# Optimization experiments

Hardware: AMD Instinct MI355X
Metric: run time of the kernel (lower is better)

The kernel has to match this reference:

```python
import jax, jax.numpy as jnp
import numpy as np

# HashGrid config (from ExplicitMaterial.Config defaults)
N_LEVELS = 16
F_PER_LEVEL = 2
TABLE_SIZE = 1 << 19          # log2_hashmap_size = 19
BASE_RES = 16
GROWTH = 1.447269237440378
N_NEURONS = 64                # VanillaMLP hidden width
N_OUT = 3                     # n_output_dims
N_POINTS = 1048576

# 8 trilinear corner offsets, [8,3]
OFFSETS = np.stack(np.meshgrid([0, 1], [0, 1], [0, 1], indexing='ij'), -1).reshape(8, 3)
PRIMES = np.array([1, 2654435761, 805459861], dtype=np.uint32)  # tcnn spatial hash primes


def _level_params():
    # tcnn convention: scale = base * growth^l - 1, resolution = ceil(scale) + 1
    out = []
    for l in range(N_LEVELS):
        scale = BASE_RES * (GROWTH ** l) - 1.0
        res = int(np.ceil(scale)) + 1
        out.append((scale, res))
    return out


def hash_grid_encode(x01, table):
    # x01: [N,3] in [0,1]; table: [L, T, F]
    offsets_u = jnp.asarray(OFFSETS, dtype=jnp.uint32)          # [8,3]
    offsets_f = jnp.asarray(OFFSETS, dtype=x01.dtype)           # [8,3]
    outs = []
    for l, (scale, res) in enumerate(_level_params()):
        pos = x01 * scale + 0.5                                  # [N,3]
        p0f = jnp.floor(pos)
        frac = pos - p0f                                         # [N,3]
        p0 = p0f.astype(jnp.uint32)
        corners = p0[:, None, :] + offsets_u                     # [N,8,3]
        if res ** 3 <= TABLE_SIZE:
            # dense indexing for coarse levels
            c = jnp.minimum(corners, np.uint32(res - 1))
            idx = c[..., 0] + c[..., 1] * np.uint32(res) + c[..., 2] * np.uint32(res * res)
        else:
            # spatial hash: xor of coordinate * prime, masked to table size
            idx = (corners[..., 0] * np.uint32(PRIMES[0])) \
                ^ (corners[..., 1] * np.uint32(PRIMES[1])) \
                ^ (corners[..., 2] * np.uint32(PRIMES[2]))
            idx = idx & np.uint32(TABLE_SIZE - 1)
        feats = table[l][idx]                                    # [N,8,F] gather
        w = jnp.prod(jnp.where(offsets_f[None] > 0, frac[:, None, :], 1.0 - frac[:, None, :]), axis=-1)  # [N,8]
        outs.append(jnp.sum(w[..., None] * feats, axis=1))       # [N,F]
    return jnp.concatenate(outs, axis=-1)                        # [N, L*F]


def setup_inputs() -> dict:
    key = jax.random.key(0)
    k1, k2, k3, k4 = jax.random.split(key, 4)
    positions = jax.random.uniform(k1, (N_POINTS, 3), dtype=jnp.float32, minval=-1.0, maxval=1.0)
    # tcnn init: uniform(-1e-4, 1e-4)
    hash_table = jax.random.uniform(k2, (N_LEVELS, TABLE_SIZE, F_PER_LEVEL), dtype=jnp.float32,
                                    minval=-1e-4, maxval=1e-4)
    d_in = N_LEVELS * F_PER_LEVEL
    w1 = jax.random.normal(k3, (d_in, N_NEURONS), dtype=jnp.float32) * (2.0 / d_in) ** 0.5
    w2 = jax.random.normal(k4, (N_NEURONS, N_OUT), dtype=jnp.float32) * (2.0 / N_NEURONS) ** 0.5
    return {"positions": positions, "hash_table": hash_table, "w1": w1, "w2": w2}


def reference(positions, hash_table, w1, w2):
    # contract_to_unisphere (bounded): scale bbox [-1,1]^3 -> [0,1]^3
    x01 = (positions + 1.0) * 0.5
    enc = hash_grid_encode(x01, hash_table)                      # [N,32]
    h = jax.nn.relu(enc @ w1)                                    # VanillaMLP, bias-free
    feat = h @ w2                                                # output_activation = none
    color = jax.nn.sigmoid(feat)                                 # material_activation
    return color
```

## Files before the change

### kernel.cpp

```cpp
#include <hip/hip_runtime.h>
#include <stdint.h>
#include <math.h>

#define NLEVELS 16
#define NDENSE  5
#define NHASH   11
#define TSIZE   (1u << 19)
#define HMASK   (TSIZE - 1u)
#define PRIME_Y 2654435761u
#define PRIME_Z 805459861u

#define FP8_SCALE 8192.0f
#define FP8_INV   (1.0f / 8192.0f)

typedef float v2f __attribute__((ext_vector_type(2)));

struct Params {
    float    scale[NLEVELS];
    unsigned res[NDENSE];
    unsigned doff[NDENSE];
    unsigned dmode;
};

__device__ __forceinline__ unsigned umin_(unsigned a, unsigned b) { return a < b ? a : b; }

__device__ __forceinline__ v2f fma2(float w, v2f f, v2f a) {
    v2f wv = {w, w};
    return __builtin_elementwise_fma(wv, f, a);
}

__global__ __launch_bounds__(256) void repack_hash8(const float4* __restrict__ src,
                                                    uint2* __restrict__ dst, int n4) {
    const int i = blockIdx.x * 256 + threadIdx.x;
    if (i >= n4) return;
    const float4 a = src[2 * i];
    const float4 b = src[2 * i + 1];
    int lo = __builtin_amdgcn_cvt_pk_fp8_f32(a.x * FP8_SCALE, a.y * FP8_SCALE, 0, false);
    lo     = __builtin_amdgcn_cvt_pk_fp8_f32(a.z * FP8_SCALE, a.w * FP8_SCALE, lo, true);
    int hi = __builtin_amdgcn_cvt_pk_fp8_f32(b.x * FP8_SCALE, b.y * FP8_SCALE, 0, false);
    hi     = __builtin_amdgcn_cvt_pk_fp8_f32(b.z * FP8_SCALE, b.w * FP8_SCALE, hi, true);
    dst[i] = make_uint2((unsigned)lo, (unsigned)hi);
}

__global__ __launch_bounds__(256) void repack_dense8(const float2* __restrict__ table,
                                                     uint2* __restrict__ dst, Params pr) {
    const int l = blockIdx.y;
    const unsigned R = pr.res[l];
    const unsigned n = R * R * R;
    const unsigned e = blockIdx.x * 256 + threadIdx.x;
    if (e >= n) return;
    const unsigned xx = e % R;
    const unsigned t  = e / R;
    const unsigned yy = t % R;
    const unsigned x1 = umin_(xx + 1u, R - 1) - xx;
    const unsigned y1 = (umin_(yy + 1u, R - 1) - yy) * R;
    const float2* src = table + (size_t)l * TSIZE;
    const float2 a = src[e];
    const float2 b = src[e + x1];
    const float2 c = src[e + y1];
    const float2 d = src[e + y1 + x1];
    int w0 = __builtin_amdgcn_cvt_pk_fp8_f32(a.x * FP8_SCALE, a.y * FP8_SCALE, 0, false);
    w0     = __builtin_amdgcn_cvt_pk_fp8_f32(b.x * FP8_SCALE, b.y * FP8_SCALE, w0, true);
    int w1 = __builtin_amdgcn_cvt_pk_fp8_f32(c.x * FP8_SCALE, c.y * FP8_SCALE, 0, false);
    w1     = __builtin_amdgcn_cvt_pk_fp8_f32(d.x * FP8_SCALE, d.y * FP8_SCALE, w1, true);
    dst[pr.doff[l] + e] = make_uint2((unsigned)w0, (unsigned)w1);
}

__global__ __launch_bounds__(256) void repack_dense16(const float2* __restrict__ table,
                                                      uint4* __restrict__ dst, Params pr) {
    const int l = blockIdx.y;
    const unsigned R = pr.res[l];
    const unsigned n = R * R * R;
    const unsigned e = blockIdx.x * 256 + threadIdx.x;
    if (e >= n) return;
    const unsigned xx = e % R;
    const unsigned t  = e / R;
    const unsigned yy = t % R;
    const unsigned zz = t / R;
    const unsigned x1 = umin_(xx + 1u, R - 1) - xx;
    const unsigned y1 = (umin_(yy + 1u, R - 1) - yy) * R;
    const unsigned z1 = (umin_(zz + 1u, R - 1) - zz) * R * R;
    const float2* src = table + (size_t)l * TSIZE;
    const float2 a0 = src[e];
    const float2 b0 = src[e + x1];
    const float2 c0 = src[e + y1];
    const float2 d0 = src[e + y1 + x1];
    const float2 a1 = src[e + z1];
    const float2 b1 = src[e + z1 + x1];
    const float2 c1 = src[e + z1 + y1];
    const float2 d1 = src[e + z1 + y1 + x1];
    int w0 = __builtin_amdgcn_cvt_pk_fp8_f32(a0.x * FP8_SCALE, a0.y * FP8_SCALE, 0, false);
    w0     = __builtin_amdgcn_cvt_pk_fp8_f32(b0.x * FP8_SCALE, b0.y * FP8_SCALE, w0, true);
    int w1 = __builtin_amdgcn_cvt_pk_fp8_f32(c0.x * FP8_SCALE, c0.y * FP8_SCALE, 0, false);
    w1     = __builtin_amdgcn_cvt_pk_fp8_f32(d0.x * FP8_SCALE, d0.y * FP8_SCALE, w1, true);
    int w2 = __builtin_amdgcn_cvt_pk_fp8_f32(a1.x * FP8_SCALE, a1.y * FP8_SCALE, 0, false);
    w2     = __builtin_amdgcn_cvt_pk_fp8_f32(b1.x * FP8_SCALE, b1.y * FP8_SCALE, w2, true);
    int w3 = __builtin_amdgcn_cvt_pk_fp8_f32(c1.x * FP8_SCALE, c1.y * FP8_SCALE, 0, false);
    w3     = __builtin_amdgcn_cvt_pk_fp8_f32(d1.x * FP8_SCALE, d1.y * FP8_SCALE, w3, true);
    uint4 o; o.x = (unsigned)w0; o.y = (unsigned)w1; o.z = (unsigned)w2; o.w = (unsigned)w3;
    dst[pr.doff[l] + e] = o;
}

__device__ __forceinline__ void lvl_tw(float x, float y, float z, float s,
                                       float* wx, float* wy, float* wz) {
    const float fx = fmaf(x, s, 0.5f), fy = fmaf(y, s, 0.5f), fz = fmaf(z, s, 0.5f);
    const float tx = fx - floorf(fx), ty = fy - floorf(fy), tz = fz - floorf(fz);
    wx[0] = 1.f - tx; wx[1] = tx;
    wy[0] = 1.f - ty; wy[1] = ty;
    wz[0] = 1.f - tz; wz[1] = tz;
}

__device__ __forceinline__ void hash_issue_pair(const void* __restrict__ hashTV, int lrel,
                                                float x, float y, float z, float s,
                                                unsigned* __restrict__ U,
                                                unsigned* __restrict__ V,
                                                unsigned* __restrict__ flg) {
    const float fx = fmaf(x, s, 0.5f), fy = fmaf(y, s, 0.5f), fz = fmaf(z, s, 0.5f);
    const unsigned x0 = (unsigned)floorf(fx);
    const unsigned y0 = (unsigned)floorf(fy);
    const unsigned z0 = (unsigned)floorf(fz);
    const unsigned hy0 = y0 * PRIME_Y, hz0 = z0 * PRIME_Z;
    unsigned H[4];
    H[0] = hy0 ^ hz0;
    H[1] = (hy0 + PRIME_Y) ^ hz0;
    H[2] = hy0 ^ (hz0 + PRIME_Z);
    H[3] = (hy0 + PRIME_Y) ^ (hz0 + PRIME_Z);
    *flg = (x0 & 1u) | (((y0 ^ z0) & 1u) << 1);
    if (x0 & 1u) {
        const unsigned short* t8 = (const unsigned short*)hashTV + (size_t)lrel * TSIZE;
#pragma unroll
        for (int c = 0; c < 4; ++c) {
            const unsigned i0 = (x0 ^ H[c]) & HMASK;
            const unsigned i1 = ((x0 + 1u) ^ H[c]) & HMASK;
            U[c] = t8[i0];
            V[c] = t8[i1];
        }
    } else {
        const unsigned* t32 = (const unsigned*)hashTV + (size_t)lrel * (TSIZE / 2);
#pragma unroll
        for (int c = 0; c < 4; ++c) {
            const unsigned i0 = (x0 ^ H[c]) & HMASK;
            U[c] = t32[i0 >> 1];
        }
    }
}

__global__ __launch_bounds__(256) void hgmlp_fp8p(
    const float* __restrict__ gpos,
    const void* __restrict__ hashTV,
    const void* __restrict__ denseTV,
    const float* __restrict__ gw1,
    const float* __restrict__ gw2,
    float* __restrict__ gout,
    int npts, Params pr)
{
    __shared__ __align__(16) float w1t[64 * 32];
    __shared__ float w2s[64 * 3];
    __shared__ __align__(16) float ostage[768];
    const int tid = threadIdx.x;
    const int p = blockIdx.x * 256 + tid;
    const bool full = (blockIdx.x * 256 + 256) <= npts;

    float px = 0.f, py = 0.f, pz = 0.f;
    if (p < npts) { px = gpos[3 * p]; py = gpos[3 * p + 1]; pz = gpos[3 * p + 2]; }

    for (int e = tid; e < 32 * 64; e += 256) {
        const int i = e & 31, j = e >> 5;
        w1t[e] = gw1[i * 64 + j] * FP8_INV;
    }
    if (tid < 192) w2s[tid] = gw2[tid];
    __syncthreads();

    const float x = (px + 1.f) * 0.5f;
    const float y = (py + 1.f) * 0.5f;
    const float z = (pz + 1.f) * 0.5f;

    v2f enc[16];

    uint4 dq[NDENSE];
#pragma unroll
    for (int l = 0; l < NDENSE; ++l) {
        const float s = pr.scale[l];
        const unsigned R = pr.res[l];
        const float fx = fmaf(x, s, 0.5f), fy = fmaf(y, s, 0.5f), fz = fmaf(z, s, 0.5f);
        const unsigned x0 = (unsigned)floorf(fx);
        const unsigned y0 = (unsigned)floorf(fy);
        const unsigned z0 = (unsigned)floorf(fz);
        const unsigned base = umin_(x0, R - 1) + umin_(y0, R - 1) * R
                            + umin_(z0, R - 1) * R * R;
        if (pr.dmode) {
            const uint4* tl = (const uint4*)denseTV + pr.doff[l];
            dq[l] = tl[base];
        } else {
            const unsigned cz1 = umin_(z0 + 1u, R - 1) * R * R - umin_(z0, R - 1) * R * R;
            const uint2* tl = (const uint2*)denseTV + pr.doff[l];
            const uint2 u0 = tl[base];
            const uint2 u1 = tl[base + cz1];
            dq[l].x = u0.x; dq[l].y = u0.y; dq[l].z = u1.x; dq[l].w = u1.y;
        }
    }

    unsigned U[4][4], V[4][4], flg[4];
    hash_issue_pair(hashTV, 0, x, y, z, pr.scale[5], U[0], V[0], &flg[0]);
    hash_issue_pair(hashTV, 1, x, y, z, pr.scale[6], U[1], V[1], &flg[1]);
    hash_issue_pair(hashTV, 2, x, y, z, pr.scale[7], U[2], V[2], &flg[2]);

#pragma unroll
    for (int l = 0; l < NDENSE; ++l) {
        float wx[2], wy[2], wz[2];
        lvl_tw(x, y, z, pr.scale[l], wx, wy, wz);
        v2f e = {0.f, 0.f};
        {
            const v2f c00 = __builtin_amdgcn_cvt_pk_f32_fp8((int)dq[l].x, false);
            const v2f c10 = __builtin_amdgcn_cvt_pk_f32_fp8((int)dq[l].x, true);
            const v2f c01 = __builtin_amdgcn_cvt_pk_f32_fp8((int)dq[l].y, false);
            const v2f c11 = __builtin_amdgcn_cvt_pk_f32_fp8((int)dq[l].y, true);
            e = fma2(wz[0] * wy[0] * wx[0], c00, e);
            e = fma2(wz[0] * wy[0] * wx[1], c10, e);
            e = fma2(wz[0] * wy[1] * wx[0], c01, e);
            e = fma2(wz[0] * wy[1] * wx[1], c11, e);
        }
        {
            const v2f c00 = __builtin_amdgcn_cvt_pk_f32_fp8((int)dq[l].z, false);
            const v2f c10 = __builtin_amdgcn_cvt_pk_f32_fp8((int)dq[l].z, true);
            const v2f c01 = __builtin_amdgcn_cvt_pk_f32_fp8((int)dq[l].w, false);
            const v2f c11 = __builtin_amdgcn_cvt_pk_f32_fp8((int)dq[l].w, true);
            e = fma2(wz[1] * wy[0] * wx[0], c00, e);
            e = fma2(wz[1] * wy[0] * wx[1], c10, e);
            e = fma2(wz[1] * wy[1] * wx[0], c01, e);
            e = fma2(wz[1] * wy[1] * wx[1], c11, e);
        }
        enc[l] = e;
    }

#pragma unroll
    for (int l = NDENSE; l < NLEVELS; ++l) {
        if (l + 3 < NLEVELS) {
            const int sl = (l + 3 - NDENSE) & 3;
            hash_issue_pair(hashTV, l + 3 - NDENSE, x, y, z, pr.scale[l + 3],
                            U[sl], V[sl], &flg[sl]);
        }
        const int sl = (l - NDENSE) & 3;
        float wx[2], wy[2], wz[2];
        lvl_tw(x, y, z, pr.scale[l], wx, wy, wz);
        const unsigned xo = flg[sl] & 1u;
        const unsigned pb = (flg[sl] >> 1) & 1u;
        v2f e = {0.f, 0.f};
#pragma unroll
        for (int c = 0; c < 4; ++c) {
            const unsigned u = U[sl][c];
            const unsigned lo = u & 0xFFFFu, hi = u >> 16;
            const unsigned swp = (xo ^ 1u) & (pb ^ (unsigned)(c & 1) ^ (unsigned)(c >> 1));
            const unsigned ec0 = xo ? lo : (swp ? hi : lo);
            const unsigned ec1 = xo ? (V[sl][c] & 0xFFFFu) : (swp ? lo : hi);
            const v2f f0 = __builtin_amdgcn_cvt_pk_f32_fp8((int)ec0, false);
            const v2f f1 = __builtin_amdgcn_cvt_pk_f32_fp8((int)ec1, false);
            const float wc = wy[c & 1] * wz[c >> 1];
            e = fma2(wc * wx[0], f0, e);
            e = fma2(wc * wx[1], f1, e);
        }
        enc[l] = e;
    }

    float o0 = 0.f, o1 = 0.f, o2 = 0.f;
#pragma unroll 4
    for (int j = 0; j < 64; ++j) {
        const float4* wr4 = (const float4*)&w1t[j * 32];
        v2f a0 = {0.f, 0.f}, a1 = {0.f, 0.f};
#pragma unroll
        for (int i = 0; i < 8; ++i) {
            const float4 w4 = wr4[i];
            const v2f wlo = {w4.x, w4.y};
            const v2f whi = {w4.z, w4.w};
            a0 = __builtin_elementwise_fma(enc[2 * i],     wlo, a0);
            a1 = __builtin_elementwise_fma(enc[2 * i + 1], whi, a1);
        }
        float acc = (a0.x + a0.y) + (a1.x + a1.y);
        acc = fmaxf(acc, 0.f);
        o0 = fmaf(acc, w2s[3 * j + 0], o0);
        o1 = fmaf(acc, w2s[3 * j + 1], o1);
        o2 = fmaf(acc, w2s[3 * j + 2], o2);
    }
    const float r0 = 1.f / (1.f + __expf(-o0));
    const float r1 = 1.f / (1.f + __expf(-o1));
    const float r2 = 1.f / (1.f + __expf(-o2));

    if (full) {
        ostage[3 * tid + 0] = r0;
        ostage[3 * tid + 1] = r1;
        ostage[3 * tid + 2] = r2;
        __syncthreads();
        if (tid < 192) {
            const float4 v = ((const float4*)ostage)[tid];
            ((float4*)(gout + (size_t)blockIdx.x * 768))[tid] = v;
        }
    } else if (p < npts) {
        gout[3 * p + 0] = r0;
        gout[3 * p + 1] = r1;
        gout[3 * p + 2] = r2;
    }
}

__global__ __launch_bounds__(256) void hgmlp_fp32(
    const float* __restrict__ gpos, const float* __restrict__ gtable,
    const float* __restrict__ gw1, const float* __restrict__ gw2,
    float* __restrict__ gout, int npts, Params pr)
{
    __shared__ float w1t[64 * 32];
    __shared__ float w2s[64 * 3];
    const int tid = threadIdx.x;
    const int p = blockIdx.x * 256 + tid;
    float px = 0.f, py = 0.f, pz = 0.f;
    if (p < npts) { px = gpos[3 * p]; py = gpos[3 * p + 1]; pz = gpos[3 * p + 2]; }
    for (int e = tid; e < 32 * 64; e += 256) { const int i = e & 31, j = e >> 5; w1t[e] = gw1[i * 64 + j]; }
    if (tid < 192) w2s[tid] = gw2[tid];
    __syncthreads();
    if (p >= npts) return;
    const float x = (px + 1.f) * 0.5f, y = (py + 1.f) * 0.5f, z = (pz + 1.f) * 0.5f;
    float enc[32];
#pragma unroll
    for (int l = 0; l < NLEVELS; ++l) {
        const float s = pr.scale[l];
        const float fx = fmaf(x, s, 0.5f), fy = fmaf(y, s, 0.5f), fz = fmaf(z, s, 0.5f);
        const float bx = floorf(fx), by = floorf(fy), bz = floorf(fz);
        const float tx = fx - bx, ty = fy - by, tz = fz - bz;
        const unsigned x0 = (unsigned)bx, y0 = (unsigned)by, z0 = (unsigned)bz;
        const float wx[2] = {1.f - tx, tx}, wy[2] = {1.f - ty, ty}, wz[2] = {1.f - tz, tz};
        const float2* tl = (const float2*)gtable + (size_t)l * TSIZE;
        float e0 = 0.f, e1 = 0.f;
        unsigned idx[8];
        if (l < NDENSE) {
            const unsigned R = pr.res[l];
            const unsigned cx[2] = {umin_(x0, R - 1), umin_(x0 + 1u, R - 1)};
            const unsigned cy[2] = {umin_(y0, R - 1) * R, umin_(y0 + 1u, R - 1) * R};
            const unsigned cz[2] = {umin_(z0, R - 1) * R * R, umin_(z0 + 1u, R - 1) * R * R};
#pragma unroll
            for (int c = 0; c < 8; ++c) idx[c] = cx[c & 1] + cy[(c >> 1) & 1] + cz[c >> 2];
        } else {
            const unsigned hy0 = y0 * PRIME_Y, hz0 = z0 * PRIME_Z;
#pragma unroll
            for (int c = 0; c < 8; ++c)
                idx[c] = ((x0 + (c & 1)) ^ (hy0 + ((c >> 1) & 1) * PRIME_Y) ^ (hz0 + (c >> 2) * PRIME_Z)) & HMASK;
        }
#pragma unroll
        for (int c = 0; c < 8; ++c) {
            const float2 f = tl[idx[c]];
            const float w = wx[c & 1] * wy[(c >> 1) & 1] * wz[c >> 2];
            e0 = fmaf(w, f.x, e0); e1 = fmaf(w, f.y, e1);
        }
        enc[2 * l + 0] = e0; enc[2 * l + 1] = e1;
    }
    float o0 = 0.f, o1 = 0.f, o2 = 0.f;
    for (int j = 0; j < 64; ++j) {
        const float* wr = &w1t[j * 32];
        float acc = 0.f;
#pragma unroll
        for (int i = 0; i < 32; ++i) acc = fmaf(enc[i], wr[i], acc);
        acc = fmaxf(acc, 0.f);
        o0 = fmaf(acc, w2s[3 * j + 0], o0);
        o1 = fmaf(acc, w2s[3 * j + 1], o1);
        o2 = fmaf(acc, w2s[3 * j + 2], o2);
    }
    gout[3 * p + 0] = 1.f / (1.f + __expf(-o0));
    gout[3 * p + 1] = 1.f / (1.f + __expf(-o1));
    gout[3 * p + 2] = 1.f / (1.f + __expf(-o2));
}

extern "C" void kernel_launch(void* const* d_in, const int* in_sizes, int n_in,
                              void* d_out, int out_size, void* d_ws, size_t ws_size,
                              hipStream_t stream)
{
    const float* gpos   = (const float*)d_in[0];
    const float* gtable = (const float*)d_in[1];
    const float* gw1    = (const float*)d_in[2];
    const float* gw2    = (const float*)d_in[3];
    float* gout = (float*)d_out;
    const int npts = in_sizes[0] / 3;

    Params pr;
    unsigned total = 0, maxn = 0;
    for (int l = 0; l < NLEVELS; ++l) {
        const double scale = 16.0 * pow(1.447269237440378, (double)l) - 1.0;
        pr.scale[l] = (float)scale;
        if (l < NDENSE) {
            const unsigned R = (unsigned)ceil(scale) + 1u;
            pr.res[l] = R;
            pr.doff[l] = total;
            total += R * R * R;
            if (R * R * R > maxn) maxn = R * R * R;
        }
    }
    const size_t hash_bytes = (size_t)NHASH * TSIZE * 2u;
    const size_t need16 = hash_bytes + (size_t)total * 16u;
    const size_t need8  = hash_bytes + (size_t)total * 8u;
    const int blocks = (npts + 255) / 256;

    if (ws_size >= need8) {
        pr.dmode = (ws_size >= need16) ? 1u : 0u;
        void* hashTV = d_ws;
        void* denseT = (char*)d_ws + hash_bytes;
        const int n4 = NHASH * TSIZE / 4;
        hipLaunchKernelGGL(repack_hash8, dim3((n4 + 255) / 256), dim3(256), 0, stream,
                           (const float4*)((const float2*)gtable + (size_t)NDENSE * TSIZE),
                           (uint2*)hashTV, n4);
        if (pr.dmode) {
            hipLaunchKernelGGL(repack_dense16, dim3((maxn + 255) / 256, NDENSE), dim3(256), 0, stream,
                               (const float2*)gtable, (uint4*)denseT, pr);
        } else {
            hipLaunchKernelGGL(repack_dense8, dim3((maxn + 255) / 256, NDENSE), dim3(256), 0, stream,
                               (const float2*)gtable, (uint2*)denseT, pr);
        }
        hipLaunchKernelGGL(hgmlp_fp8p, dim3(blocks), dim3(256), 0, stream,
                           gpos, hashTV, denseT, gw1, gw2, gout, npts, pr);
    } else {
        hipLaunchKernelGGL(hgmlp_fp32, dim3(blocks), dim3(256), 0, stream,
                           gpos, gtable, gw1, gw2, gout, npts, pr);
    }
}
```

Baseline: 354.6 us.

## Compute first MLP layer with bf16 MFMA via LDS-staged encodings

Replaces the per-thread scalar FP32 64x32 matmul with MFMA 16x16x32 bf16 instructions. Each wave stages its bf16-packed encodings in LDS, loads W1 as bf16 fragments, and then does the ReLU, the W2 projection and cross-lane reductions via shuffles before the sigmoid. This removes most of the VALU FMA work, at the cost of extra LDS traffic, lower precision (bf16 inputs) and more shared memory per block, which may reduce occupancy.

```diff
diff --git a/kernel.cpp b/kernel.cpp
--- a/kernel.cpp
+++ b/kernel.cpp
@@ -14,6 +14,10 @@
 #define FP8_INV   (1.0f / 8192.0f)
 
 typedef float v2f __attribute__((ext_vector_type(2)));
+typedef short bf16x8 __attribute__((ext_vector_type(8)));
+typedef float f32x4 __attribute__((ext_vector_type(4)));
+typedef unsigned int uint;
+typedef unsigned short ushort;
 
 struct Params {
     float    scale[NLEVELS];
@@ -154,9 +158,11 @@
     float* __restrict__ gout,
     int npts, Params pr)
 {
-    __shared__ __align__(16) float w1t[64 * 32];
-    __shared__ float w2s[64 * 3];
-    __shared__ __align__(16) float ostage[768];
+    __shared__ __align__(16) ushort w1tb[64 * 40];
+    __shared__ __align__(16) float  w2s4[64 * 4];
+    __shared__ __align__(16) ushort encT[4 * 64 * 40];
+    __shared__ __align__(16) float  ostage[768];
+
     const int tid = threadIdx.x;
     const int p = blockIdx.x * 256 + tid;
     const bool full = (blockIdx.x * 256 + 256) <= npts;
@@ -164,11 +170,16 @@
     float px = 0.f, py = 0.f, pz = 0.f;
     if (p < npts) { px = gpos[3 * p]; py = gpos[3 * p + 1]; pz = gpos[3 * p + 2]; }
 
-    for (int e = tid; e < 32 * 64; e += 256) {
-        const int i = e & 31, j = e >> 5;
-        w1t[e] = gw1[i * 64 + j] * FP8_INV;
-    }
-    if (tid < 192) w2s[tid] = gw2[tid];
+    for (int t = tid; t < 1024; t += 256) {
+        const int n = t >> 4, j = t & 15;
+        const float v0 = gw1[(2 * j)     * 64 + n] * FP8_INV;
+        const float v1 = gw1[(2 * j + 1) * 64 + n] * FP8_INV;
+        uint u;
+        asm("v_cvt_pk_bf16_f32 %0, %1, %2" : "=v"(u) : "v"(v0), "v"(v1));
+        ((uint*)w1tb)[n * 20 + j] = u;
+    }
+    if (tid < 192) w2s4[(tid / 3) * 4 + (tid % 3)] = gw2[tid];
+    if (tid < 64)  w2s4[tid * 4 + 3] = 0.f;
     __syncthreads();
 
     const float x = (px + 1.f) * 0.5f;
@@ -262,42 +273,100 @@
         enc[l] = e;
     }
 
-    float o0 = 0.f, o1 = 0.f, o2 = 0.f;
-#pragma unroll 4
-    for (int j = 0; j < 64; ++j) {
-        const float4* wr4 = (const float4*)&w1t[j * 32];
-        v2f a0 = {0.f, 0.f}, a1 = {0.f, 0.f};
-#pragma unroll
-        for (int i = 0; i < 8; ++i) {
-            const float4 w4 = wr4[i];
-            const v2f wlo = {w4.x, w4.y};
-            const v2f whi = {w4.z, w4.w};
-            a0 = __builtin_elementwise_fma(enc[2 * i],     wlo, a0);
-            a1 = __builtin_elementwise_fma(enc[2 * i + 1], whi, a1);
-        }
-        float acc = (a0.x + a0.y) + (a1.x + a1.y);
-        acc = fmaxf(acc, 0.f);
-        o0 = fmaf(acc, w2s[3 * j + 0], o0);
-        o1 = fmaf(acc, w2s[3 * j + 1], o1);
-        o2 = fmaf(acc, w2s[3 * j + 2], o2);
-    }
-    const float r0 = 1.f / (1.f + __expf(-o0));
-    const float r1 = 1.f / (1.f + __expf(-o1));
-    const float r2 = 1.f / (1.f + __expf(-o2));
+    const int lane = tid & 63;
+    const int wv   = tid >> 6;
+    const int lr   = lane & 15;
+    const int lg   = lane >> 4;
+
+    {
+        uint pk[16];
+#pragma unroll
+        for (int i = 0; i < 16; ++i) {
+            const float ex = enc[i].x, ey = enc[i].y;
+            uint u;
+            asm("v_cvt_pk_bf16_f32 %0, %1, %2" : "=v"(u) : "v"(ex), "v"(ey));
+            pk[i] = u;
+        }
+        uint* rowu = (uint*)&encT[(wv * 64 + lane) * 40];
+#pragma unroll
+        for (int j = 0; j < 4; ++j) {
+            uint4 q; q.x = pk[4 * j]; q.y = pk[4 * j + 1];
+            q.z = pk[4 * j + 2]; q.w = pk[4 * j + 3];
+            *(uint4*)(rowu + 4 * j) = q;
+        }
+    }
+
+    f32x4 acc[4][4];
+#pragma unroll
+    for (int a = 0; a < 4; ++a)
+#pragma unroll
+        for (int b = 0; b < 4; ++b)
+            acc[a][b] = (f32x4){0.f, 0.f, 0.f, 0.f};
+
+    bf16x8 bfr[4];
+#pragma unroll
+    for (int pg = 0; pg < 4; ++pg)
+        bfr[pg] = *(const bf16x8*)((const char*)encT +
+                     (size_t)(wv * 64 + pg * 16 + lr) * 80 + (size_t)lg * 16);
+#pragma unroll
+    for (int ng = 0; ng < 4; ++ng) {
+        const bf16x8 afr = *(const bf16x8*)((const char*)w1tb +
+                     (size_t)(ng * 16 + lr) * 80 + (size_t)lg * 16);
+#pragma unroll
+        for (int pg = 0; pg < 4; ++pg)
+            acc[ng][pg] = __builtin_amdgcn_mfma_f32_16x16x32_bf16(afr, bfr[pg],
+                                                                  acc[ng][pg], 0, 0, 0);
+    }
+
+    float po[4][3];
+#pragma unroll
+    for (int pg = 0; pg < 4; ++pg) { po[pg][0] = 0.f; po[pg][1] = 0.f; po[pg][2] = 0.f; }
+#pragma unroll
+    for (int ng = 0; ng < 4; ++ng) {
+#pragma unroll
+        for (int i = 0; i < 4; ++i) {
+            const int n = ng * 16 + lg * 4 + i;
+            const float4 wv2 = *(const float4*)&w2s4[n * 4];
+#pragma unroll
+            for (int pg = 0; pg < 4; ++pg) {
+                const float h = fmaxf(acc[ng][pg][i], 0.f);
+                po[pg][0] = fmaf(h, wv2.x, po[pg][0]);
+                po[pg][1] = fmaf(h, wv2.y, po[pg][1]);
+                po[pg][2] = fmaf(h, wv2.z, po[pg][2]);
+            }
+        }
+    }
+#pragma unroll
+    for (int pg = 0; pg < 4; ++pg)
+#pragma unroll
+        for (int c = 0; c < 3; ++c) {
+            float v = po[pg][c];
+            v += __shfl_xor(v, 16);
+            v += __shfl_xor(v, 32);
+            po[pg][c] = v;
+        }
+
+    if (lg == 0) {
+#pragma unroll
+        for (int pg = 0; pg < 4; ++pg) {
+            const int pt = wv * 64 + pg * 16 + lr;
+            ostage[pt * 3 + 0] = 1.f / (1.f + __expf(-po[pg][0]));
+            ostage[pt * 3 + 1] = 1.f / (1.f + __expf(-po[pg][1]));
+            ostage[pt * 3 + 2] = 1.f / (1.f + __expf(-po[pg][2]));
+        }
+    }
+    __syncthreads();
 
     if (full) {
-        ostage[3 * tid + 0] = r0;
-        ostage[3 * tid + 1] = r1;
-        ostage[3 * tid + 2] = r2;
-        __syncthreads();
         if (tid < 192) {
             const float4 v = ((const float4*)ostage)[tid];
             ((float4*)(gout + (size_t)blockIdx.x * 768))[tid] = v;
         }
-    } else if (p < npts) {
-        gout[3 * p + 0] = r0;
-        gout[3 * p + 1] = r1;
-        gout[3 * p + 2] = r2;
+    } else {
+        for (int e = tid; e < 768; e += 256) {
+            const int gidx = blockIdx.x * 768 + e;
+            if (gidx < npts * 3) gout[gidx] = ostage[e];
+        }
     }
 }
 
```

Result: faster. 345.6 us (median of 2 runs) (-2.5%).
